# Kernel optimization log

Hardware: AMD Instinct MI355X
Metric: run time of the kernel (lower is better)

Reference implementation:

```python
import jax, jax.numpy as jnp
import numpy as np

D_MODEL = 1024
N_HEADS = 16
D_HEAD = D_MODEL // N_HEADS
LN_EPS = 1e-5


def setup_inputs() -> dict:
    key = jax.random.key(0)
    ks = jax.random.split(key, 10)
    B, N = 2, 2048
    s = 1.0 / np.sqrt(D_MODEL)
    return {
        "x": jax.random.normal(ks[0], (B, N, D_MODEL), dtype=jnp.float32),
        "Wq": jax.random.normal(ks[1], (D_MODEL, D_MODEL), dtype=jnp.float32) * s,
        "bq": jnp.zeros((D_MODEL,), dtype=jnp.float32),
        "Wk": jax.random.normal(ks[2], (D_MODEL, D_MODEL), dtype=jnp.float32) * s,
        "bk": jnp.zeros((D_MODEL,), dtype=jnp.float32),
        "Wv": jax.random.normal(ks[3], (D_MODEL, D_MODEL), dtype=jnp.float32) * s,
        "bv": jnp.zeros((D_MODEL,), dtype=jnp.float32),
        "Wo": jax.random.normal(ks[4], (D_MODEL, D_MODEL), dtype=jnp.float32) * s,
        "bo": jnp.zeros((D_MODEL,), dtype=jnp.float32),
        "ln_gamma": jnp.ones((D_MODEL,), dtype=jnp.float32),
        "ln_beta": jnp.zeros((D_MODEL,), dtype=jnp.float32),
    }


def reference(x, Wq, bq, Wk, bk, Wv, bv, Wo, bo, ln_gamma, ln_beta):
    B, N, _ = x.shape
    # QKV projections -> [B, H, N, dh]
    def proj(W, b):
        return (x @ W.T + b).reshape(B, N, N_HEADS, D_HEAD).transpose(0, 2, 1, 3)
    Q, K, V = proj(Wq, bq), proj(Wk, bk), proj(Wv, bv)
    # scaled scores [B, H, N, N] with causal mask (is_mask=True)
    scores = jnp.einsum("bhqd,bhkd->bhqk", Q, K) / np.sqrt(D_HEAD)
    causal = jnp.tril(jnp.ones((N, N), dtype=bool))
    scores = jnp.where(causal, scores, -jnp.inf)
    attn = jax.nn.softmax(scores, axis=-1)  # dropout p=0 (eval)
    ctx = jnp.einsum("bhqk,bhkd->bhqd", attn, V)  # [B, H, N, dh]
    ctx = ctx.transpose(0, 2, 1, 3).reshape(B, N, D_MODEL)
    out = ctx @ Wo.T + bo + x  # output proj + residual
    # LayerNorm over last dim
    mu = out.mean(-1, keepdims=True)
    var = out.var(-1, keepdims=True)
    return (out - mu) / jnp.sqrt(var + LN_EPS) * ln_gamma + ln_beta
```

## Files before the change

kernel.cpp:

```cpp
#include <hip/hip_runtime.h>
#include <type_traits>

#define D_MODEL 1024
#define NHEADS 16
#define DHEAD 64
#define SEQ 2048
#define BATCH 2
#define MROWS (BATCH*SEQ)
#define NQT (SEQ/64)

typedef unsigned short ushort_t;
typedef unsigned int   u32;
using bf16x8 = __attribute__((ext_vector_type(8))) __bf16;
using bf16x4 = __attribute__((ext_vector_type(4))) __bf16;
using us4    = __attribute__((ext_vector_type(4))) unsigned short;
using us8    = __attribute__((ext_vector_type(8))) unsigned short;
using f32x4  = __attribute__((ext_vector_type(4))) float;
using f32x2  = __attribute__((ext_vector_type(2))) float;

#define QSCALE 0.18033688011112042f

__device__ __forceinline__ float fast_exp2(float x) {
#if __has_builtin(__builtin_amdgcn_exp2f)
    return __builtin_amdgcn_exp2f(x);
#else
    return __expf(x * 0.6931471805599453f);
#endif
}

__device__ __forceinline__ void gl2lds(const ushort_t* g, ushort_t* l) {
    __builtin_amdgcn_global_load_lds(
        (const __attribute__((address_space(1))) unsigned int*)g,
        (__attribute__((address_space(3))) unsigned int*)l,
        16, 0, 0);
}

__global__ __launch_bounds__(256) void cvt_kernel(
    const float* __restrict__ x,
    const float* __restrict__ wq, const float* __restrict__ wk,
    const float* __restrict__ wv, const float* __restrict__ wo,
    ushort_t* __restrict__ xb,
    ushort_t* __restrict__ wqb, ushort_t* __restrict__ wkb,
    ushort_t* __restrict__ wvb, ushort_t* __restrict__ wob)
{
    const size_t XN = (size_t)MROWS * D_MODEL;
    const size_t WN = (size_t)D_MODEL * D_MODEL;
    size_t i = ((size_t)blockIdx.x * 256 + threadIdx.x) * 8;
    const float* s; ushort_t* d; size_t off;
    if (i < XN) { s = x; d = xb; off = i; }
    else {
        size_t j = i - XN;
        int w = (int)(j / WN);
        off = j - (size_t)w * WN;
        s = (w == 0) ? wq : (w == 1) ? wk : (w == 2) ? wv : wo;
        d = (w == 0) ? wqb : (w == 1) ? wkb : (w == 2) ? wvb : wob;
    }
    const f32x4 v0 = *(const f32x4*)(s + off);
    const f32x4 v1 = *(const f32x4*)(s + off + 4);
    bf16x8 o;
    #pragma unroll
    for (int t = 0; t < 4; ++t) o[t] = (__bf16)v0[t];
    #pragma unroll
    for (int t = 0; t < 4; ++t) o[4 + t] = (__bf16)v1[t];
    *(bf16x8*)(d + off) = o;
}

template<typename OutT, bool RES, int BM, int BN>
__global__ __launch_bounds__(256, 3) void gemm_nt(
    const ushort_t* __restrict__ A,
    const ushort_t* __restrict__ W0, const ushort_t* __restrict__ W1, const ushort_t* __restrict__ W2,
    const float* __restrict__ b0, const float* __restrict__ b1, const float* __restrict__ b2,
    const float* __restrict__ res,
    OutT* __restrict__ Y0, OutT* __restrict__ Y1, OutT* __restrict__ Y2,
    float qsc)
{
    constexpr int K  = D_MODEL;
    constexpr int MR = BM / 32;
    constexpr int NR = BN / 32;
    constexpr int CA = BM / 64;
    constexpr int CW = BN / 64;
    __shared__ ushort_t As[2][BM * 32];
    __shared__ ushort_t Ws[2][BN * 32];

    const int z = blockIdx.z;
    const ushort_t* W  = (z == 0) ? W0 : (z == 1) ? W1 : W2;
    const float* bias  = (z == 0) ? b0 : (z == 1) ? b1 : b2;
    OutT* Y            = (z == 0) ? Y0 : (z == 1) ? Y1 : Y2;
    const float sc     = (z == 0) ? qsc : 1.0f;

    const int i0 = blockIdx.x * BM;
    const int j0 = blockIdx.y * BN;
    const int tid  = threadIdx.x;
    const int lane = tid & 63;
    const int w    = tid >> 6;
    const int wm   = (w >> 1) * (BM / 2);
    const int wn   = (w & 1) * (BN / 2);
    const int l15  = lane & 15;
    const int quad = lane >> 4;

    const int srow = lane >> 2;
    const int scol = ((lane & 3) ^ ((lane >> 3) & 3)) * 8;
    const ushort_t* gA[CA];
    const ushort_t* gW[CW];
    #pragma unroll
    for (int c = 0; c < CA; ++c)
        gA[c] = A + (size_t)(i0 + (w * CA + c) * 16 + srow) * K + scol;
    #pragma unroll
    for (int c = 0; c < CW; ++c)
        gW[c] = W + (size_t)(j0 + (w * CW + c) * 16 + srow) * K + scol;

    const int rc = (quad ^ ((l15 >> 1) & 3)) * 8;

    f32x4 acc[MR][NR] = {};

    for (int k0 = 0; k0 < K; k0 += 64) {
        #pragma unroll
        for (int c = 0; c < CA; ++c) {
            gl2lds(gA[c] + k0,      &As[0][(w * CA + c) * 512]);
            gl2lds(gA[c] + k0 + 32, &As[1][(w * CA + c) * 512]);
        }
        #pragma unroll
        for (int c = 0; c < CW; ++c) {
            gl2lds(gW[c] + k0,      &Ws[0][(w * CW + c) * 512]);
            gl2lds(gW[c] + k0 + 32, &Ws[1][(w * CW + c) * 512]);
        }
        __syncthreads();

        #pragma unroll
        for (int s = 0; s < 2; ++s) {
            bf16x8 af[MR], wf[NR];
            #pragma unroll
            for (int m = 0; m < MR; ++m)
                af[m] = *(const bf16x8*)&As[s][(wm + m * 16 + l15) * 32 + rc];
            #pragma unroll
            for (int n = 0; n < NR; ++n)
                wf[n] = *(const bf16x8*)&Ws[s][(wn + n * 16 + l15) * 32 + rc];
            #pragma unroll
            for (int m = 0; m < MR; ++m)
                #pragma unroll
                for (int n = 0; n < NR; ++n)
                    acc[m][n] = __builtin_amdgcn_mfma_f32_16x16x32_bf16(wf[n], af[m], acc[m][n], 0, 0, 0);
        }
        __syncthreads();
    }

    #pragma unroll
    for (int n = 0; n < NR; ++n) {
        const int col = j0 + wn + n * 16 + quad * 4;
        const f32x4 bv = *(const f32x4*)&bias[col];
        #pragma unroll
        for (int m = 0; m < MR; ++m) {
            const int row = i0 + wm + m * 16 + l15;
            if constexpr (std::is_same<OutT, float>::value) {
                f32x4 v;
                #pragma unroll
                for (int r = 0; r < 4; ++r) v[r] = acc[m][n][r] + bv[r];
                if constexpr (RES) {
                    const f32x4 rv = *(const f32x4*)&res[(size_t)row * D_MODEL + col];
                    #pragma unroll
                    for (int r = 0; r < 4; ++r) v[r] += rv[r];
                }
                *(f32x4*)&Y[(size_t)row * D_MODEL + col] = v;
            } else {
                bf16x4 pk;
                #pragma unroll
                for (int r = 0; r < 4; ++r) pk[r] = (__bf16)((acc[m][n][r] + bv[r]) * sc);
                *(bf16x4*)&Y[(size_t)row * D_MODEL + col] = pk;
            }
        }
    }
}

#define KD 64

__global__ __launch_bounds__(256, 3) void attn_kernel(
    const ushort_t* __restrict__ Qg, const ushort_t* __restrict__ Kg,
    const ushort_t* __restrict__ Vg, ushort_t* __restrict__ Og,
    float* __restrict__ wso, float* __restrict__ wsml)
{
    __shared__ __align__(16) ushort_t Kt[2][64 * KD];
    __shared__ __align__(16) ushort_t Vt[2][64 * KD];
    __shared__ __align__(16) ushort_t Pw[128 * KD];

    const int bh = blockIdx.x;
    const int b = bh >> 4;
    const int h = bh & 15;

    const int y = blockIdx.y;
    int qp, kt0, kt1, part;
    bool heavy;
    if (y < 16) {
        const int t = y & 7;
        qp = 15 - t;
        part = y >> 3;
        const int nkt = 2 * qp + 2;
        const int hh = qp + 1;
        heavy = true;
        if (part) { kt0 = hh; kt1 = nkt; }
        else      { kt0 = 0;  kt1 = hh;  }
    } else {
        qp = y - 16;
        part = 0;
        kt0 = 0; kt1 = 2 * qp + 2;
        heavy = false;
    }
    const int qtL = 2 * qp;
    const int qtU = 2 * qp + 1;
    const int q0 = qp * 128;

    const int tid  = threadIdx.x;
    const int lane = tid & 63;
    const int w    = tid >> 6;
    const int l15  = lane & 15;
    const int quad = lane >> 4;

    const size_t headoff = (size_t)h * DHEAD;
    const ushort_t* Kbase = Kg + (size_t)(b * SEQ) * D_MODEL + headoff;
    const ushort_t* Vbase = Vg + (size_t)(b * SEQ) * D_MODEL + headoff;

    const int krow = tid >> 3;
    const int kb   = tid & 7;
    const int vkey = tid & 63;
    const int dc0  = tid >> 6;
    const int dc1  = dc0 + 4;

    const int rx = (l15 & 7) << 3;
    const int cs0 = (quad * 8) ^ rx;
    const int cs1 = (32 + quad * 8) ^ rx;
    int pwc[4];
    #pragma unroll
    for (int f = 0; f < 4; ++f) pwc[f] = (f * 16 + quad * 4) ^ rx;
    ushort_t* PwRowL = &Pw[(w * 16 + l15) * KD];
    ushort_t* PwRowU = &Pw[(64 + w * 16 + l15) * KD];

    const int kwa = krow * KD + ((kb * 8) ^ ((krow & 7) << 3));

    const int qgL = q0 + w * 16 + l15;
    const int qgU = q0 + 64 + w * 16 + l15;
    const size_t qrowL = (size_t)(b * SEQ + qgL) * D_MODEL + headoff;
    const size_t qrowU = (size_t)(b * SEQ + qgU) * D_MODEL + headoff;
    const bf16x8 qf0L = *(const bf16x8*)&Qg[qrowL + quad * 8];
    const bf16x8 qf1L = *(const bf16x8*)&Qg[qrowL + 32 + quad * 8];
    const bf16x8 qf0U = *(const bf16x8*)&Qg[qrowU + quad * 8];
    const bf16x8 qf1U = *(const bf16x8*)&Qg[qrowU + 32 + quad * 8];

    bf16x8 onesf;
    #pragma unroll
    for (int j = 0; j < 8; ++j) onesf[j] = (__bf16)1.0f;

    float m_runL = -1e30f, m_runU = -1e30f;
    f32x4 oL[4] = {}, oU[4] = {};
    f32x4 o4L = {}, o4U = {};

    us8 kp0, kp1, vp0, vp1;
    const size_t koff0 = (size_t)(kt0 * 64) * D_MODEL;
    kp0 = *(const us8*)&Kbase[koff0 + (size_t)krow * D_MODEL + kb * 8];
    kp1 = *(const us8*)&Kbase[koff0 + (size_t)(32 + krow) * D_MODEL + kb * 8];
    vp0 = *(const us8*)&Vbase[koff0 + (size_t)vkey * D_MODEL + dc0 * 8];
    vp1 = *(const us8*)&Vbase[koff0 + (size_t)vkey * D_MODEL + dc1 * 8];
    *(us8*)&Kt[0][kwa]           = kp0;
    *(us8*)&Kt[0][kwa + 32 * KD] = kp1;
    #pragma unroll
    for (int j = 0; j < 8; ++j) {
        Vt[0][(dc0 * 8 + j) * KD + (vkey ^ (j << 3))] = vp0[j];
        Vt[0][(dc1 * 8 + j) * KD + (vkey ^ (j << 3))] = vp1[j];
    }
    __syncthreads();

    for (int kt = kt0; kt < kt1; ++kt) {
        const int cur = (kt - kt0) & 1;
        const int nxt = cur ^ 1;
        const bool pre = (kt + 1 < kt1);
        const bool actL = (kt <= qtL);
        if (pre) {
            const size_t koff = (size_t)((kt + 1) * 64) * D_MODEL;
            kp0 = *(const us8*)&Kbase[koff + (size_t)krow * D_MODEL + kb * 8];
            kp1 = *(const us8*)&Kbase[koff + (size_t)(32 + krow) * D_MODEL + kb * 8];
            vp0 = *(const us8*)&Vbase[koff + (size_t)vkey * D_MODEL + dc0 * 8];
            vp1 = *(const us8*)&Vbase[koff + (size_t)vkey * D_MODEL + dc1 * 8];
        }

        f32x4 svL[4], svU[4];
        __builtin_amdgcn_s_setprio(1);
        #pragma unroll
        for (int f = 0; f < 4; ++f) {
            const int rbase = (f * 16 + l15) * KD;
            const bf16x8 kf0 = *(const bf16x8*)&Kt[cur][rbase + cs0];
            const bf16x8 kf1 = *(const bf16x8*)&Kt[cur][rbase + cs1];
            f32x4 sU = {};
            sU = __builtin_amdgcn_mfma_f32_16x16x32_bf16(kf0, qf0U, sU, 0, 0, 0);
            sU = __builtin_amdgcn_mfma_f32_16x16x32_bf16(kf1, qf1U, sU, 0, 0, 0);
            svU[f] = sU;
            f32x4 sL = {};
            sL = __builtin_amdgcn_mfma_f32_16x16x32_bf16(kf0, qf0L, sL, 0, 0, 0);
            sL = __builtin_amdgcn_mfma_f32_16x16x32_bf16(kf1, qf1L, sL, 0, 0, 0);
            svL[f] = sL;
        }
        __builtin_amdgcn_s_setprio(0);

        if (kt == qtU) {
            #pragma unroll
            for (int f = 0; f < 4; ++f)
                #pragma unroll
                for (int r = 0; r < 4; ++r) {
                    const int kg = kt * 64 + f * 16 + quad * 4 + r;
                    svU[f][r] = (kg <= qgU) ? svU[f][r] : -1e30f;
                }
        }
        if (kt == qtL) {
            #pragma unroll
            for (int f = 0; f < 4; ++f)
                #pragma unroll
                for (int r = 0; r < 4; ++r) {
                    const int kg = kt * 64 + f * 16 + quad * 4 + r;
                    svL[f][r] = (kg <= qgL) ? svL[f][r] : -1e30f;
                }
        }

        {
            float mf[4];
            #pragma unroll
            for (int f = 0; f < 4; ++f)
                mf[f] = fmaxf(fmaxf(svU[f][0], svU[f][1]), fmaxf(svU[f][2], svU[f][3]));
            float mx = fmaxf(fmaxf(mf[0], mf[1]), fmaxf(mf[2], mf[3]));
            mx = fmaxf(mx, __shfl_xor(mx, 16));
            mx = fmaxf(mx, __shfl_xor(mx, 32));
            if (!__all(mx <= m_runU + 8.0f)) {
                const float mn = fmaxf(m_runU, mx);
                const float al = fast_exp2(m_runU - mn);
                m_runU = mn;
                #pragma unroll
                for (int t = 0; t < 4; ++t)
                    #pragma unroll
                    for (int r = 0; r < 4; ++r) oU[t][r] *= al;
                o4U[0] *= al;
            }
            #pragma unroll
            for (int f = 0; f < 4; ++f) {
                bf16x4 pk;
                #pragma unroll
                for (int r = 0; r < 4; ++r)
                    pk[r] = (__bf16)fast_exp2(svU[f][r] - m_runU);
                *(bf16x4*)&PwRowU[pwc[f]] = pk;
            }
        }
        if (actL) {
            float mf[4];
            #pragma unroll
            for (int f = 0; f < 4; ++f)
                mf[f] = fmaxf(fmaxf(svL[f][0], svL[f][1]), fmaxf(svL[f][2], svL[f][3]));
            float mx = fmaxf(fmaxf(mf[0], mf[1]), fmaxf(mf[2], mf[3]));
            mx = fmaxf(mx, __shfl_xor(mx, 16));
            mx = fmaxf(mx, __shfl_xor(mx, 32));
            if (!__all(mx <= m_runL + 8.0f)) {
                const float mn = fmaxf(m_runL, mx);
                const float al = fast_exp2(m_runL - mn);
                m_runL = mn;
                #pragma unroll
                for (int t = 0; t < 4; ++t)
                    #pragma unroll
                    for (int r = 0; r < 4; ++r) oL[t][r] *= al;
                o4L[0] *= al;
            }
            #pragma unroll
            for (int f = 0; f < 4; ++f) {
                bf16x4 pk;
                #pragma unroll
                for (int r = 0; r < 4; ++r)
                    pk[r] = (__bf16)fast_exp2(svL[f][r] - m_runL);
                *(bf16x4*)&PwRowL[pwc[f]] = pk;
            }
        }
        __asm__ volatile("s_waitcnt lgkmcnt(0)" ::: "memory");

        __builtin_amdgcn_s_setprio(1);
        #pragma unroll
        for (int s = 0; s < 2; ++s) {
            const int cc = s ? cs1 : cs0;
            const bf16x8 pfU = *(const bf16x8*)&PwRowU[cc];
            if (actL) {
                const bf16x8 pfL = *(const bf16x8*)&PwRowL[cc];
                #pragma unroll
                for (int t = 0; t < 4; ++t) {
                    const bf16x8 vf = *(const bf16x8*)&Vt[cur][(t * 16 + l15) * KD + cc];
                    oU[t] = __builtin_amdgcn_mfma_f32_16x16x32_bf16(vf, pfU, oU[t], 0, 0, 0);
                    oL[t] = __builtin_amdgcn_mfma_f32_16x16x32_bf16(vf, pfL, oL[t], 0, 0, 0);
                }
                o4U = __builtin_amdgcn_mfma_f32_16x16x32_bf16(onesf, pfU, o4U, 0, 0, 0);
                o4L = __builtin_amdgcn_mfma_f32_16x16x32_bf16(onesf, pfL, o4L, 0, 0, 0);
            } else {
                #pragma unroll
                for (int t = 0; t < 4; ++t) {
                    const bf16x8 vf = *(const bf16x8*)&Vt[cur][(t * 16 + l15) * KD + cc];
                    oU[t] = __builtin_amdgcn_mfma_f32_16x16x32_bf16(vf, pfU, oU[t], 0, 0, 0);
                }
                o4U = __builtin_amdgcn_mfma_f32_16x16x32_bf16(onesf, pfU, o4U, 0, 0, 0);
            }
        }
        __builtin_amdgcn_s_setprio(0);

        if (pre) {
            *(us8*)&Kt[nxt][kwa]           = kp0;
            *(us8*)&Kt[nxt][kwa + 32 * KD] = kp1;
            #pragma unroll
            for (int j = 0; j < 8; ++j) {
                Vt[nxt][(dc0 * 8 + j) * KD + (vkey ^ (j << 3))] = vp0[j];
                Vt[nxt][(dc1 * 8 + j) * KD + (vkey ^ (j << 3))] = vp1[j];
            }
        }
        __asm__ volatile("s_waitcnt lgkmcnt(0)\n\ts_barrier" ::: "memory");
    }

    if (!heavy) {
        const float invL = 1.f / o4L[0];
        const float invU = 1.f / o4U[0];
        const size_t orowL = (size_t)(b * SEQ + qgL) * D_MODEL + headoff;
        const size_t orowU = (size_t)(b * SEQ + qgU) * D_MODEL + headoff;
        #pragma unroll
        for (int t = 0; t < 4; ++t) {
            bf16x4 pkL, pkU;
            #pragma unroll
            for (int r = 0; r < 4; ++r) {
                pkL[r] = (__bf16)(oL[t][r] * invL);
                pkU[r] = (__bf16)(oU[t][r] * invU);
            }
            *(bf16x4*)&Og[orowL + t * 16 + quad * 4] = pkL;
            *(bf16x4*)&Og[orowU + t * 16 + quad * 4] = pkU;
        }
    } else {
        const int T = (bh * 8 + (qp - 8)) * 2 + part;
        const int rL = w * 16 + l15;
        const int rU = 64 + w * 16 + l15;
        float* wo = wso + (size_t)T * 8192;
        #pragma unroll
        for (int t = 0; t < 4; ++t) {
            *(f32x4*)&wo[(size_t)rL * 64 + t * 16 + quad * 4] = oL[t];
            *(f32x4*)&wo[(size_t)rU * 64 + t * 16 + quad * 4] = oU[t];
        }
        if (quad == 0) {
            f32x2 mlL = { m_runL, o4L[0] };
            f32x2 mlU = { m_runU, o4U[0] };
            *(f32x2*)&wsml[(size_t)(T * 128 + rL) * 2] = mlL;
            *(f32x2*)&wsml[(size_t)(T * 128 + rU) * 2] = mlU;
        }
    }
}

__global__ __launch_bounds__(256) void attn_combine(
    const float* __restrict__ wso, const float* __restrict__ wsml,
    ushort_t* __restrict__ Og)
{
    const int gid = blockIdx.x * 256 + threadIdx.x;
    const int row = gid >> 4;
    const int dp  = (gid & 15) * 4;
    const int bh  = row >> 10;
    const int rr  = row & 1023;
    const int qph = rr >> 7;
    const int q   = rr & 127;
    const int T0  = (bh * 8 + qph) * 2;

    const f32x2 ml0 = *(const f32x2*)&wsml[(size_t)(T0 * 128 + q) * 2];
    const f32x2 ml1 = *(const f32x2*)&wsml[(size_t)((T0 + 1) * 128 + q) * 2];
    const float M  = fmaxf(ml0[0], ml1[0]);
    const float a0 = fast_exp2(ml0[0] - M);
    const float a1 = fast_exp2(ml1[0] - M);
    const float inv = 1.0f / (ml0[1] * a0 + ml1[1] * a1);

    const f32x4 o0 = *(const f32x4*)&wso[(size_t)T0 * 8192 + q * 64 + dp];
    const f32x4 o1 = *(const f32x4*)&wso[(size_t)(T0 + 1) * 8192 + q * 64 + dp];

    const int b = bh >> 4;
    const int h = bh & 15;
    const int qg = 1024 + rr;
    bf16x4 pk;
    #pragma unroll
    for (int r = 0; r < 4; ++r)
        pk[r] = (__bf16)((o0[r] * a0 + o1[r] * a1) * inv);
    *(bf16x4*)&Og[(size_t)(b * SEQ + qg) * D_MODEL + h * DHEAD + dp] = pk;
}

__global__ __launch_bounds__(256) void ln_kernel(
    const float* __restrict__ X, const float* __restrict__ g,
    const float* __restrict__ bta, float* __restrict__ out)
{
    __shared__ float r1[4], r2[4];
    const int row = blockIdx.x;
    const int tid = threadIdx.x;
    const float* p = X + (size_t)row * D_MODEL;
    float v[4]; float s1 = 0.f, s2 = 0.f;
    #pragma unroll
    for (int i = 0; i < 4; ++i) { v[i] = p[tid + 256 * i]; s1 += v[i]; s2 += v[i] * v[i]; }
    #pragma unroll
    for (int d = 32; d >= 1; d >>= 1) { s1 += __shfl_xor(s1, d); s2 += __shfl_xor(s2, d); }
    if ((tid & 63) == 0) { r1[tid >> 6] = s1; r2[tid >> 6] = s2; }
    __syncthreads();
    s1 = r1[0] + r1[1] + r1[2] + r1[3];
    s2 = r2[0] + r2[1] + r2[2] + r2[3];
    const float mu  = s1 * (1.f / D_MODEL);
    const float var = s2 * (1.f / D_MODEL) - mu * mu;
    const float rstd = rsqrtf(var + 1e-5f);
    #pragma unroll
    for (int i = 0; i < 4; ++i) {
        const int c = tid + 256 * i;
        out[(size_t)row * D_MODEL + c] = (v[i] - mu) * rstd * g[c] + bta[c];
    }
}

extern "C" void kernel_launch(void* const* d_in, const int* in_sizes, int n_in,
                              void* d_out, int out_size, void* d_ws, size_t ws_size,
                              hipStream_t stream) {
    const float* x     = (const float*)d_in[0];
    const float* Wq    = (const float*)d_in[1];
    const float* bq    = (const float*)d_in[2];
    const float* Wk    = (const float*)d_in[3];
    const float* bk    = (const float*)d_in[4];
    const float* Wv    = (const float*)d_in[5];
    const float* bv    = (const float*)d_in[6];
    const float* Wo    = (const float*)d_in[7];
    const float* bo    = (const float*)d_in[8];
    const float* gamma = (const float*)d_in[9];
    const float* beta  = (const float*)d_in[10];

    const size_t XN = (size_t)MROWS * D_MODEL;
    const size_t WN = (size_t)D_MODEL * D_MODEL;
    ushort_t* wsp = (ushort_t*)d_ws;
    ushort_t* xb  = wsp;
    ushort_t* Yq  = wsp + XN;
    ushort_t* Yk  = wsp + 2 * XN;
    ushort_t* Yv  = wsp + 3 * XN;
    ushort_t* Wqb = wsp + 4 * XN;
    ushort_t* Wkb = Wqb + WN;
    ushort_t* Wvb = Wkb + WN;
    ushort_t* Wob = Wvb + WN;
    ushort_t* ctx = xb;
    float*    pre = (float*)d_out;

    float* wso  = (float*)(wsp + 4 * XN + 4 * WN);
    float* wsml = wso + (size_t)512 * 8192;

    cvt_kernel<<<dim3(4096), 256, 0, stream>>>(x, Wq, Wk, Wv, Wo, xb, Wqb, Wkb, Wvb, Wob);

    gemm_nt<ushort_t, false, 128, 128><<<dim3(MROWS / 128, D_MODEL / 128, 3), 256, 0, stream>>>(
        xb, Wqb, Wkb, Wvb, bq, bk, bv, nullptr, Yq, Yk, Yv, QSCALE);

    attn_kernel<<<dim3(BATCH * NHEADS, 24), 256, 0, stream>>>(Yq, Yk, Yv, ctx, wso, wsml);

    attn_combine<<<dim3(2048), 256, 0, stream>>>(wso, wsml, ctx);

    gemm_nt<float, true, 64, 128><<<dim3(MROWS / 64, D_MODEL / 128, 1), 256, 0, stream>>>(
        ctx, Wob, Wob, Wob, bo, bo, bo, x, pre, pre, pre, 1.0f);

    ln_kernel<<<dim3(MROWS), 256, 0, stream>>>(pre, gamma, beta, (float*)d_out);
}
```

Before: 194.9 us.

## Rebalance causal attention split-KV partitioning with 2- and 3-way splits

```diff
diff --git a/kernel.cpp b/kernel.cpp
--- a/kernel.cpp
+++ b/kernel.cpp
@@ -186,24 +186,21 @@
     const int b = bh >> 4;
     const int h = bh & 15;
 
-    const int y = blockIdx.y;
-    int qp, kt0, kt1, part;
-    bool heavy;
-    if (y < 16) {
-        const int t = y & 7;
-        qp = 15 - t;
-        part = y >> 3;
-        const int nkt = 2 * qp + 2;
-        const int hh = qp + 1;
-        heavy = true;
-        if (part) { kt0 = hh; kt1 = nkt; }
-        else      { kt0 = 0;  kt1 = hh;  }
-    } else {
-        qp = y - 16;
-        part = 0;
-        kt0 = 0; kt1 = 2 * qp + 2;
-        heavy = false;
-    }
+    static const unsigned char ymap[30] = {
+        61, 56, 60, 36, 37, 32, 44, 20,
+        62, 57, 49, 52, 53, 33, 45, 40,
+        54, 58, 50, 12, 28, 29, 16, 41,
+         0,  4,  8, 24, 25, 48
+    };
+    const int v    = ymap[blockIdx.y];
+    const int qp   = v >> 2;
+    const int part = v & 3;
+    const int P    = (qp < 6) ? 1 : (qp < 12) ? 2 : 3;
+    const int N    = 2 * qp + 2;
+    const int kt0  = part * N / P;
+    const int kt1  = (part + 1) * N / P;
+    const bool heavy = (P > 1);
+
     const int qtL = 2 * qp;
     const int qtU = 2 * qp + 1;
     const int q0 = qp * 128;
@@ -428,7 +425,8 @@
             *(bf16x4*)&Og[orowU + t * 16 + quad * 4] = pkU;
         }
     } else {
-        const int T = (bh * 8 + (qp - 8)) * 2 + part;
+        const int c = (qp < 12) ? (qp - 6) * 2 + part : 12 + (qp - 12) * 3 + part;
+        const int T = bh * 24 + c;
         const int rL = w * 16 + l15;
         const int rU = 64 + w * 16 + l15;
         float* wo = wso + (size_t)T * 8192;
@@ -450,32 +448,40 @@
     const float* __restrict__ wso, const float* __restrict__ wsml,
     ushort_t* __restrict__ Og)
 {
+    const int bh  = blockIdx.y;
     const int gid = blockIdx.x * 256 + threadIdx.x;
-    const int row = gid >> 4;
+    const int rib = gid >> 4;
     const int dp  = (gid & 15) * 4;
-    const int bh  = row >> 10;
-    const int rr  = row & 1023;
-    const int qph = rr >> 7;
-    const int q   = rr & 127;
-    const int T0  = (bh * 8 + qph) * 2;
-
-    const f32x2 ml0 = *(const f32x2*)&wsml[(size_t)(T0 * 128 + q) * 2];
-    const f32x2 ml1 = *(const f32x2*)&wsml[(size_t)((T0 + 1) * 128 + q) * 2];
-    const float M  = fmaxf(ml0[0], ml1[0]);
-    const float a0 = fast_exp2(ml0[0] - M);
-    const float a1 = fast_exp2(ml1[0] - M);
-    const float inv = 1.0f / (ml0[1] * a0 + ml1[1] * a1);
-
-    const f32x4 o0 = *(const f32x4*)&wso[(size_t)T0 * 8192 + q * 64 + dp];
-    const f32x4 o1 = *(const f32x4*)&wso[(size_t)(T0 + 1) * 8192 + q * 64 + dp];
+    const int pi  = rib >> 7;
+    const int q   = rib & 127;
+    const int qp  = 6 + pi;
+    const int P   = (qp < 12) ? 2 : 3;
+    const int c0  = (qp < 12) ? (qp - 6) * 2 : 12 + (qp - 12) * 3;
+    const int T0  = bh * 24 + c0;
+
+    const f32x2 mlA = *(const f32x2*)&wsml[(size_t)((T0 + 0) * 128 + q) * 2];
+    const f32x2 mlB = *(const f32x2*)&wsml[(size_t)((T0 + 1) * 128 + q) * 2];
+    f32x2 mlC = { -1e30f, 0.f };
+    if (P == 3) mlC = *(const f32x2*)&wsml[(size_t)((T0 + 2) * 128 + q) * 2];
+
+    const float M  = fmaxf(fmaxf(mlA[0], mlB[0]), mlC[0]);
+    const float aA = fast_exp2(mlA[0] - M);
+    const float aB = fast_exp2(mlB[0] - M);
+    const float aC = fast_exp2(mlC[0] - M);
+    const float inv = 1.0f / (mlA[1] * aA + mlB[1] * aB + mlC[1] * aC);
+
+    const f32x4 oA = *(const f32x4*)&wso[(size_t)(T0 + 0) * 8192 + q * 64 + dp];
+    const f32x4 oB = *(const f32x4*)&wso[(size_t)(T0 + 1) * 8192 + q * 64 + dp];
+    f32x4 oC = {};
+    if (P == 3) oC = *(const f32x4*)&wso[(size_t)(T0 + 2) * 8192 + q * 64 + dp];
 
     const int b = bh >> 4;
     const int h = bh & 15;
-    const int qg = 1024 + rr;
+    const int qg = qp * 128 + q;
     bf16x4 pk;
     #pragma unroll
     for (int r = 0; r < 4; ++r)
-        pk[r] = (__bf16)((o0[r] * a0 + o1[r] * a1) * inv);
+        pk[r] = (__bf16)((oA[r] * aA + oB[r] * aB + oC[r] * aC) * inv);
     *(bf16x4*)&Og[(size_t)(b * SEQ + qg) * D_MODEL + h * DHEAD + dp] = pk;
 }
 
@@ -536,16 +542,16 @@
     float*    pre = (float*)d_out;
 
     float* wso  = (float*)(wsp + 4 * XN + 4 * WN);
-    float* wsml = wso + (size_t)512 * 8192;
+    float* wsml = wso + (size_t)768 * 8192;
 
     cvt_kernel<<<dim3(4096), 256, 0, stream>>>(x, Wq, Wk, Wv, Wo, xb, Wqb, Wkb, Wvb, Wob);
 
     gemm_nt<ushort_t, false, 128, 128><<<dim3(MROWS / 128, D_MODEL / 128, 3), 256, 0, stream>>>(
         xb, Wqb, Wkb, Wvb, bq, bk, bv, nullptr, Yq, Yk, Yv, QSCALE);
 
-    attn_kernel<<<dim3(BATCH * NHEADS, 24), 256, 0, stream>>>(Yq, Yk, Yv, ctx, wso, wsml);
-
-    attn_combine<<<dim3(2048), 256, 0, stream>>>(wso, wsml, ctx);
+    attn_kernel<<<dim3(BATCH * NHEADS, 30), 256, 0, stream>>>(Yq, Yk, Yv, ctx, wso, wsml);
+
+    attn_combine<<<dim3(80, 32), 256, 0, stream>>>(wso, wsml, ctx);
 
     gemm_nt<float, true, 64, 128><<<dim3(MROWS / 64, D_MODEL / 128, 1), 256, 0, stream>>>(
         ctx, Wob, Wob, Wob, bo, bo, bo, x, pre, pre, pre, 1.0f);
```

Result: no change. 198.6 us (+1.9%).
